# Kernel tuning notes

Measured on AMD Instinct MI355X. Metric: run time of the kernel, lower is better.

The kernel has to match this reference:

```python
import jax, jax.numpy as jnp
import numpy as np

NUM_NODES = 100000
NUM_RELATIONS = 16
HIDDEN = 64
NUM_LAYERS = 3
NUM_EDGES = 1600000


def setup_inputs() -> dict:
    key = jax.random.key(0)
    ks = jax.random.split(key, 6)
    edge_index = jax.random.randint(ks[0], (2, NUM_EDGES), 0, NUM_NODES, dtype=jnp.int64 if jax.config.jax_enable_x64 else jnp.int32)
    edge_type = jax.random.randint(ks[1], (NUM_EDGES,), 0, NUM_RELATIONS, dtype=edge_index.dtype)
    scale = 1.0 / np.sqrt(HIDDEN)
    node_emb = jax.random.normal(ks[2], (NUM_NODES, HIDDEN), dtype=jnp.float32) * scale
    # Per-layer relation weights [L, R, d, h], root weights [L, d, h], bias [L, h]
    W = jax.random.normal(ks[3], (NUM_LAYERS, NUM_RELATIONS, HIDDEN, HIDDEN), dtype=jnp.float32) * scale
    W_root = jax.random.normal(ks[4], (NUM_LAYERS, HIDDEN, HIDDEN), dtype=jnp.float32) * scale
    bias = jnp.zeros((NUM_LAYERS, HIDDEN), dtype=jnp.float32)
    return {"edge_index": edge_index, "edge_type": edge_type,
            "node_emb": node_emb, "W": W, "W_root": W_root, "bias": bias}


def _rgcn_layer(x, src, dst, et, Wr, Wroot, b):
    # PyG RGCNConv: out_i = W_root x_i + b + sum_r (1/|N_r(i)|) sum_{j in N_r(i)} W_r x_j
    N, d = x.shape
    R = Wr.shape[0]
    # Transform all nodes by every relation weight: [R, N, h] (dense grouped GEMM)
    xW = jnp.einsum('nd,rdh->rnh', x, Wr)
    m = xW[et, src]                      # [E, h] per-edge messages (gather)
    seg = dst * R + et                   # joint (dst, relation) segment id
    counts = jax.ops.segment_sum(jnp.ones((m.shape[0],), dtype=x.dtype), seg, num_segments=N * R)
    norm = 1.0 / jnp.maximum(counts, 1.0)
    m = m * norm[seg][:, None]           # per-relation mean normalization
    agg = jax.ops.segment_sum(m, dst, num_segments=N)  # scatter-add over dst
    return agg + x @ Wroot + b


def reference(edge_index, edge_type, node_emb, W, W_root, bias):
    src, dst = edge_index[0], edge_index[1]
    x = node_emb  # note: Embedding.max_norm only applies on index lookups; .weight used raw here
    n_layers = W.shape[0]
    for i in range(n_layers):
        x = _rgcn_layer(x, src, dst, edge_type, W[i], W_root[i], bias[i])
        if i < n_layers - 1:
            x = jax.nn.relu(x)
    return x
```

## Files before the change

kernel.cpp:

```cpp
#include <hip/hip_runtime.h>


#define HID   64
#define NREL  16
#define KD    1088
#define NPB   16
#define NPW   2
#define LSTR  1096

#define NBKT  1024
#define BSH   7
#define FB    2048
#define CAPB  4096
#define CHA   8192

typedef __attribute__((ext_vector_type(8))) short bf16x8;
typedef __attribute__((ext_vector_type(4))) float f32x4;
typedef unsigned short us16;
typedef unsigned int u32;

__device__ __forceinline__ float b2f(us16 u) {
    union { u32 i; float f; } c; c.i = ((u32)u) << 16; return c.f;
}
__device__ __forceinline__ us16 f2b(float f) {
    union { float f; u32 i; } c; c.f = f;
    u32 x = c.i;
    return (us16)((x + 0x7FFFu + ((x >> 16) & 1u)) >> 16);
}


__global__ __launch_bounds__(256) void bucket_count(const int* __restrict__ ei,
                                                    int* __restrict__ counts_b, int E) {
    __shared__ int h[NBKT];
    const int t = threadIdx.x;
    for (int i = t; i < NBKT; i += 256) h[i] = 0;
    __syncthreads();
    const int* dstp = ei + E;
    int start = blockIdx.x * CHA, end = min(start + CHA, E);
    for (int e4 = start + t * 4; e4 < end; e4 += 1024) {
        if (e4 + 3 < end) {
            int4 d = *(const int4*)(dstp + e4);
            atomicAdd(&h[d.x >> BSH], 1);
            atomicAdd(&h[d.y >> BSH], 1);
            atomicAdd(&h[d.z >> BSH], 1);
            atomicAdd(&h[d.w >> BSH], 1);
        } else {
            for (int e = e4; e < end; ++e) atomicAdd(&h[dstp[e] >> BSH], 1);
        }
    }
    __syncthreads();
    for (int i = t; i < NBKT; i += 256) {
        int v = h[i];
        if (v) atomicAdd(&counts_b[i], v);
    }
}

__global__ __launch_bounds__(NBKT) void scan_buckets(const int* __restrict__ counts_b,
                                                     int* __restrict__ bucket_base,
                                                     int* __restrict__ cursor_b,
                                                     int* __restrict__ row_ptr,
                                                     int N, int E) {
    __shared__ int s[NBKT];
    int t = threadIdx.x;
    int v = counts_b[t];
    s[t] = v; __syncthreads();
    for (int off = 1; off < NBKT; off <<= 1) {
        int tv = (t >= off) ? s[t - off] : 0;
        __syncthreads();
        s[t] += tv;
        __syncthreads();
    }
    int ex = s[t] - v;
    bucket_base[t] = ex;
    cursor_b[t] = ex;
    if (t == NBKT - 1) bucket_base[NBKT] = ex + v;
    if (t == 0) row_ptr[N] = E;
}

__global__ __launch_bounds__(256) void bucket_place(const int* __restrict__ ei,
                                                    const int* __restrict__ et,
                                                    int* __restrict__ cursor_b,
                                                    u32* __restrict__ packed, int E) {
    __shared__ int cnt[NBKT];
    __shared__ int bse[NBKT];
    const int t = threadIdx.x;
    for (int i = t; i < NBKT; i += 256) cnt[i] = 0;
    __syncthreads();
    const int* dstp = ei + E;
    int start = blockIdx.x * CHA, end = min(start + CHA, E);
    for (int e4 = start + t * 4; e4 < end; e4 += 1024) {
        if (e4 + 3 < end) {
            int4 d = *(const int4*)(dstp + e4);
            atomicAdd(&cnt[d.x >> BSH], 1);
            atomicAdd(&cnt[d.y >> BSH], 1);
            atomicAdd(&cnt[d.z >> BSH], 1);
            atomicAdd(&cnt[d.w >> BSH], 1);
        } else {
            for (int e = e4; e < end; ++e) atomicAdd(&cnt[dstp[e] >> BSH], 1);
        }
    }
    __syncthreads();
    for (int i = t; i < NBKT; i += 256) {
        int v = cnt[i];
        bse[i] = v ? atomicAdd(&cursor_b[i], v) : 0;
        cnt[i] = 0;
    }
    __syncthreads();
    #define PLACE1(sv, dv, tv)                                            \
        { int b_ = (dv) >> BSH;                                           \
          int r_ = atomicAdd(&cnt[b_], 1);                                \
          packed[bse[b_] + r_] = (u32)(sv) | ((u32)(tv) << 17)            \
                               | ((u32)((dv) & 127) << 21); }
    for (int e4 = start + t * 4; e4 < end; e4 += 1024) {
        if (e4 + 3 < end) {
            int4 sv = *(const int4*)(ei + e4);
            int4 dv = *(const int4*)(dstp + e4);
            int4 tv = *(const int4*)(et + e4);
            PLACE1(sv.x, dv.x, tv.x);
            PLACE1(sv.y, dv.y, tv.y);
            PLACE1(sv.z, dv.z, tv.z);
            PLACE1(sv.w, dv.w, tv.w);
        } else {
            for (int e = e4; e < end; ++e) PLACE1(ei[e], dstp[e], et[e]);
        }
    }
    #undef PLACE1
}

__global__ __launch_bounds__(256) void bucket_sort(const u32* __restrict__ packed,
                                                   const int* __restrict__ bucket_base,
                                                   u32* __restrict__ md,
                                                   int* __restrict__ row_ptr, int N) {
    __shared__ int hist[FB];
    __shared__ int ss[256];
    __shared__ u32 outb[CAPB];
    const int b = blockIdx.x, t = threadIdx.x;
    const int base = bucket_base[b];
    const int cnt = bucket_base[b + 1] - base;

    for (int i = t; i < FB; i += 256) hist[i] = 0;
    __syncthreads();
    for (int i = t; i < cnt; i += 256) {
        u32 p = packed[base + i];
        int f = (int)(((p >> 21) & 127u) * 16u + ((p >> 17) & 15u));
        atomicAdd(&hist[f], 1);
    }
    __syncthreads();
    int loc[8], s = 0;
    #pragma unroll
    for (int j = 0; j < 8; ++j) { loc[j] = hist[t * 8 + j]; s += loc[j]; }
    ss[t] = s; __syncthreads();
    for (int off = 1; off < 256; off <<= 1) {
        int tv = (t >= off) ? ss[t - off] : 0;
        __syncthreads();
        ss[t] += tv;
        __syncthreads();
    }
    int run = ss[t] - s;
    #pragma unroll
    for (int j = 0; j < 8; ++j) { hist[t * 8 + j] = run; run += loc[j]; }
    __syncthreads();
    if (t < 128) {
        int node = b * 128 + t;
        if (node < N) row_ptr[node] = base + hist[t * 16];
    }
    __syncthreads();
    for (int i = t; i < cnt; i += 256) {
        u32 p = packed[base + i];
        int f = (int)(((p >> 21) & 127u) * 16u + ((p >> 17) & 15u));
        int pos = atomicAdd(&hist[f], 1);
        u32 v = (p & 0x1FFFFu) | (((p >> 17) & 15u) << 20);
        if (pos < CAPB) outb[pos] = v;
        else            md[base + pos] = v;
    }
    __syncthreads();
    for (int i = t; i < cnt && i < CAPB; i += 256)
        md[base + i] = outb[i];
}

__global__ void convx_kernel(const float* __restrict__ x, us16* __restrict__ xb, int n4) {
    int i = blockIdx.x * 256 + threadIdx.x;
    if (i < n4) {
        float4 v = ((const float4*)x)[i];
        us16* o = xb + i * 4;
        o[0] = f2b(v.x); o[1] = f2b(v.y); o[2] = f2b(v.z); o[3] = f2b(v.w);
    }
}

__global__ void convw_kernel(const float* __restrict__ W, const float* __restrict__ Wroot,
                             us16* __restrict__ WcatT, int total, int L) {
    int i = blockIdx.x * 256 + threadIdx.x;
    if (i < total) {
        int l = i / (HID * KD);
        int rem = i % (HID * KD);
        int h = rem / KD, k = rem % KD;
        float v;
        if (k < NREL * HID) {
            int r = k >> 6, d = k & 63;
            v = W[(((size_t)l * NREL + r) * HID + d) * HID + h];
        } else {
            int d = k - NREL * HID;
            v = Wroot[((size_t)l * HID + d) * HID + h];
        }
        WcatT[i] = f2b(v);
    }
}


__device__ __forceinline__ void proc_window(
        u32 p_l, int c0, int wcnt, const us16* __restrict__ x_in, us16* Hrow, int lane,
        float& acc, int& runlen, int& prev, u32& mask)
{
    #pragma unroll 1
    for (int c = c0; c < wcnt; c += 16) {
        us16 hv[16]; int pe[16];
        #pragma unroll
        for (int j = 0; j < 16; ++j) {
            int idx = c + j; if (idx >= wcnt) idx = wcnt - 1;
            pe[j] = __builtin_amdgcn_readlane((int)p_l, idx);
            hv[j] = x_in[((u32)pe[j] & 0xFFFFFu) * HID + lane];
        }
        int m = wcnt - c; if (m > 16) m = 16;
        #pragma unroll
        for (int j = 0; j < 16; ++j) {
            if (j < m) {
                int r = (int)(((u32)pe[j]) >> 20);
                if (r != prev) {
                    if (prev >= 0) {
                        Hrow[(prev << 6) + lane] =
                            f2b(acc * __builtin_amdgcn_rcpf((float)runlen));
                        mask |= 1u << prev;
                    }
                    prev = r; acc = 0.f; runlen = 0;
                }
                acc += b2f(hv[j]); ++runlen;
            }
        }
    }
}

__global__ __launch_bounds__(512, 8) void layer_kernel(
        const us16* __restrict__ x_in,
        const int*  __restrict__ row_ptr,
        const u32*  __restrict__ md,
        const us16* __restrict__ WcatT,
        const float* __restrict__ bias,
        us16* __restrict__ x_out,
        float* __restrict__ out_f32,
        int flags, int N)
{
    __shared__ us16 H[NPB * LSTR];
    const int tid = threadIdx.x, wave = tid >> 6, lane = tid & 63;
    const int node0 = blockIdx.x * NPB;
    const int nodeq = node0 + wave * NPW;

    int rp[NPW + 1];
    #pragma unroll
    for (int i = 0; i <= NPW; ++i)
        rp[i] = __builtin_amdgcn_readfirstlane(row_ptr[min(nodeq + i, N)]);

    u32 pl[NPW]; us16 xr[NPW];
    #pragma unroll
    for (int q = 0; q < NPW; ++q) {
        int cnt = rp[q + 1] - rp[q];
        pl[q] = (lane < cnt) ? md[rp[q] + lane] : 0;
        xr[q] = (nodeq + q < N) ? x_in[(nodeq + q) * HID + lane] : (us16)0;
    }

    #pragma unroll
    for (int q = 0; q < NPW; ++q) {
        int node = nodeq + q;
        if (node >= N) break;
        int start = rp[q], cnt = rp[q + 1] - start;
        us16* Hrow = H + (wave * NPW + q) * LSTR;
        Hrow[NREL * HID + lane] = xr[q];

        float acc = 0.f;
        int runlen = 0, prev = -1;
        u32 mask = 0;

        proc_window(pl[q], 0, min(cnt, 64), x_in, Hrow, lane, acc, runlen, prev, mask);
        for (int w0 = 64; w0 < cnt; w0 += 64) {
            int wcnt = min(64, cnt - w0);
            u32 p2 = (lane < wcnt) ? md[start + w0 + lane] : 0;
            proc_window(p2, 0, wcnt, x_in, Hrow, lane, acc, runlen, prev, mask);
        }
        if (prev >= 0) {
            Hrow[(prev << 6) + lane] = f2b(acc * __builtin_amdgcn_rcpf((float)runlen));
            mask |= 1u << prev;
        }
        #pragma unroll
        for (int r = 0; r < NREL; ++r)
            if (!(mask & (1u << r))) Hrow[(r << 6) + lane] = 0;
    }
    __syncthreads();

    if (wave < 4) {
        const int n16 = lane & 15, quad = lane >> 4;
        f32x4 acc = {0.f, 0.f, 0.f, 0.f};
        const us16* Abase = H + n16 * LSTR + quad * 8;
        const us16* Bbase = WcatT + (size_t)(wave * 16 + n16) * KD + quad * 8;
        #pragma unroll 2
        for (int ks = 0; ks < KD / 32; ++ks) {
            bf16x8 af = *(const bf16x8*)(Abase + ks * 32);
            bf16x8 bf = *(const bf16x8*)(Bbase + ks * 32);
            acc = __builtin_amdgcn_mfma_f32_16x16x32_bf16(af, bf, acc, 0, 0, 0);
        }

        int col = wave * 16 + n16;
        float bv = bias[col];
        #pragma unroll
        for (int ri = 0; ri < 4; ++ri) {
            int nl = quad * 4 + ri, node = node0 + nl;
            if (node < N) {
                float v = acc[ri] + bv;
                if (flags & 1) v = fmaxf(v, 0.f);
                if (flags & 2) out_f32[node * HID + col] = v;
                else           x_out [node * HID + col] = f2b(v);
            }
        }
    }
}


extern "C" void kernel_launch(void* const* d_in, const int* in_sizes, int n_in,
                              void* d_out, int out_size, void* d_ws, size_t ws_size,
                              hipStream_t stream) {
    const int*   edge_index = (const int*)  d_in[0];
    const int*   edge_type  = (const int*)  d_in[1];
    const float* node_emb   = (const float*)d_in[2];
    const float* W          = (const float*)d_in[3];
    const float* Wroot      = (const float*)d_in[4];
    const float* bias       = (const float*)d_in[5];
    float* out = (float*)d_out;

    const int E = in_sizes[1];
    const int N = in_sizes[2] / HID;
    const int L = in_sizes[5] / HID;

    char* p = (char*)d_ws;
    size_t off = 0;
    auto carve = [&](size_t bytes) {
        void* q = p + off;
        off = (off + bytes + 255) & ~(size_t)255;
        return q;
    };
    int*   counts_b    = (int*)  carve((size_t)NBKT * 4);
    int*   bucket_base = (int*)  carve((size_t)(NBKT + 1) * 4);
    int*   cursor_b    = (int*)  carve((size_t)NBKT * 4);
    int*   row_ptr     = (int*)  carve((size_t)(N + 1) * 4);
    u32*   packed      = (u32*)  carve((size_t)E * 4);
    u32*   md          = (u32*)  carve((size_t)E * 4);
    us16*  xb0         = (us16*) carve((size_t)N * HID * 2);
    us16*  xb1         = (us16*) carve((size_t)N * HID * 2);
    us16*  WcatT       = (us16*) carve((size_t)L * HID * KD * 2);
    (void)ws_size; (void)n_in; (void)out_size;

    hipMemsetAsync(counts_b, 0, (size_t)NBKT * 4, stream);

    const int nblkA = (E + CHA - 1) / CHA;
    bucket_count<<<nblkA, 256, 0, stream>>>(edge_index, counts_b, E);
    scan_buckets<<<1, NBKT, 0, stream>>>(counts_b, bucket_base, cursor_b, row_ptr, N, E);
    bucket_place<<<nblkA, 256, 0, stream>>>(edge_index, edge_type, cursor_b, packed, E);
    bucket_sort<<<(N + 127) / 128, 256, 0, stream>>>(packed, bucket_base, md, row_ptr, N);

    convx_kernel<<<(N * HID / 4 + 255) / 256, 256, 0, stream>>>(node_emb, xb0, N * HID / 4);
    int wtot = L * HID * KD;
    convw_kernel<<<(wtot + 255) / 256, 256, 0, stream>>>(W, Wroot, WcatT, wtot, L);

    int gl = (N + NPB - 1) / NPB;
    us16* xin = xb0;
    us16* xother = xb1;
    for (int l = 0; l < L; ++l) {
        int last = (l == L - 1);
        int flags = (last ? 2 : 1);
        layer_kernel<<<gl, 512, 0, stream>>>(
            xin, row_ptr, md,
            WcatT + (size_t)l * HID * KD, bias + (size_t)l * HID,
            last ? nullptr : xother, last ? out : nullptr,
            flags, N);
        us16* t = xin; xin = xother; xother = t;
    }
}
```

Measured before the change: 535.0 us.

## Dynamically assign nodes to waves via shared-memory atomic work queue

Replaces the static two-nodes-per-wave assignment in the gather phase with a per-block LDS atomic counter. Each wave grabs the next node index and prefetches the following node's metadata and root row while it aggregates the current one. The goal is to balance uneven node degrees across the eight waves so the block waits less at the barrier before the MFMA stage. The cost is an extra barrier plus per-node LDS atomics and shuffles, and unrolled independent loads are traded for a software-pipelined loop.

```diff
diff --git a/kernel.cpp b/kernel.cpp
--- a/kernel.cpp
+++ b/kernel.cpp
@@ -5,7 +5,6 @@
 #define NREL  16
 #define KD    1088
 #define NPB   16
-#define NPW   2
 #define LSTR  1096
 
 #define NBKT  1024
@@ -250,48 +249,72 @@
         int flags, int N)
 {
     __shared__ us16 H[NPB * LSTR];
+    __shared__ int rp_s[NPB + 1];
+    __shared__ int qctr;
     const int tid = threadIdx.x, wave = tid >> 6, lane = tid & 63;
     const int node0 = blockIdx.x * NPB;
-    const int nodeq = node0 + wave * NPW;
-
-    int rp[NPW + 1];
-    #pragma unroll
-    for (int i = 0; i <= NPW; ++i)
-        rp[i] = __builtin_amdgcn_readfirstlane(row_ptr[min(nodeq + i, N)]);
-
-    u32 pl[NPW]; us16 xr[NPW];
-    #pragma unroll
-    for (int q = 0; q < NPW; ++q) {
-        int cnt = rp[q + 1] - rp[q];
-        pl[q] = (lane < cnt) ? md[rp[q] + lane] : 0;
-        xr[q] = (nodeq + q < N) ? x_in[(nodeq + q) * HID + lane] : (us16)0;
-    }
-
-    #pragma unroll
-    for (int q = 0; q < NPW; ++q) {
-        int node = nodeq + q;
-        if (node >= N) break;
-        int start = rp[q], cnt = rp[q + 1] - start;
-        us16* Hrow = H + (wave * NPW + q) * LSTR;
-        Hrow[NREL * HID + lane] = xr[q];
-
-        float acc = 0.f;
-        int runlen = 0, prev = -1;
-        u32 mask = 0;
-
-        proc_window(pl[q], 0, min(cnt, 64), x_in, Hrow, lane, acc, runlen, prev, mask);
-        for (int w0 = 64; w0 < cnt; w0 += 64) {
-            int wcnt = min(64, cnt - w0);
-            u32 p2 = (lane < wcnt) ? md[start + w0 + lane] : 0;
-            proc_window(p2, 0, wcnt, x_in, Hrow, lane, acc, runlen, prev, mask);
-        }
-        if (prev >= 0) {
-            Hrow[(prev << 6) + lane] = f2b(acc * __builtin_amdgcn_rcpf((float)runlen));
-            mask |= 1u << prev;
-        }
-        #pragma unroll
-        for (int r = 0; r < NREL; ++r)
-            if (!(mask & (1u << r))) Hrow[(r << 6) + lane] = 0;
+
+    if (tid <= NPB) rp_s[tid] = row_ptr[min(node0 + tid, N)];
+    if (tid == 0) qctr = 0;
+    __syncthreads();
+
+    {
+        int cA = 0;
+        if (lane == 0) cA = atomicAdd(&qctr, 1);
+        cA = __shfl(cA, 0);
+        int sA = 0, eA = 0; u32 plA = 0; us16 xrA = 0;
+        if (cA < NPB) {
+            sA = rp_s[cA]; eA = rp_s[cA + 1];
+            sA = __builtin_amdgcn_readfirstlane(sA);
+            eA = __builtin_amdgcn_readfirstlane(eA);
+            int cnt = eA - sA;
+            plA = (lane < cnt) ? md[sA + lane] : 0;
+            xrA = (node0 + cA < N) ? x_in[(size_t)(node0 + cA) * HID + lane] : (us16)0;
+        }
+
+        while (cA < NPB) {
+            int cB = 0;
+            if (lane == 0) cB = atomicAdd(&qctr, 1);
+            cB = __shfl(cB, 0);
+            int sB = 0, eB = 0; u32 plB = 0; us16 xrB = 0;
+            if (cB < NPB) {
+                sB = rp_s[cB]; eB = rp_s[cB + 1];
+                sB = __builtin_amdgcn_readfirstlane(sB);
+                eB = __builtin_amdgcn_readfirstlane(eB);
+                int cnt = eB - sB;
+                plB = (lane < cnt) ? md[sB + lane] : 0;
+                xrB = (node0 + cB < N) ? x_in[(size_t)(node0 + cB) * HID + lane] : (us16)0;
+            }
+
+            if (node0 + cA < N) {
+                int start = sA, cnt = eA - sA;
+                us16* Hrow = H + cA * LSTR;
+                Hrow[NREL * HID + lane] = xrA;
+
+                float acc = 0.f;
+                int runlen = 0, prev = -1;
+                u32 mask = 0;
+
+                proc_window(plA, 0, min(cnt, 64), x_in, Hrow, lane,
+                            acc, runlen, prev, mask);
+                for (int w0 = 64; w0 < cnt; w0 += 64) {
+                    int wcnt = min(64, cnt - w0);
+                    u32 p2 = (lane < wcnt) ? md[start + w0 + lane] : 0;
+                    proc_window(p2, 0, wcnt, x_in, Hrow, lane,
+                                acc, runlen, prev, mask);
+                }
+                if (prev >= 0) {
+                    Hrow[(prev << 6) + lane] =
+                        f2b(acc * __builtin_amdgcn_rcpf((float)runlen));
+                    mask |= 1u << prev;
+                }
+                #pragma unroll
+                for (int r = 0; r < NREL; ++r)
+                    if (!(mask & (1u << r))) Hrow[(r << 6) + lane] = 0;
+            }
+
+            cA = cB; sA = sB; eA = eB; plA = plB; xrA = xrB;
+        }
     }
     __syncthreads();
 
```

After: 569.3 us. 6.4% more time.

## Drop the bucket counting pass by placing edges into fixed-capacity buckets

Applied to the files above, without the earlier changes.

Removes the separate bucket_count kernel. Each of the 1024 buckets now gets a fixed 4096-slot region, so bucket_place can scatter packed edges directly, and the per-bucket cursors double as counts. The prefix scan runs after placement to produce compact bucket bases for bucket_sort. This saves one full read of the destination array and one launch, but uses a larger scratch buffer and silently overflows if any 128-node bucket receives more than 4096 edges, which only holds for fairly uniform graphs.

```diff
diff --git a/kernel.cpp b/kernel.cpp
--- a/kernel.cpp
+++ b/kernel.cpp
@@ -10,6 +10,7 @@
 
 #define NBKT  1024
 #define BSH   7
+#define BCAP  4096
 #define FB    2048
 #define CAPB  4096
 #define CHA   8192
@@ -28,54 +29,6 @@
     return (us16)((x + 0x7FFFu + ((x >> 16) & 1u)) >> 16);
 }
 
-
-__global__ __launch_bounds__(256) void bucket_count(const int* __restrict__ ei,
-                                                    int* __restrict__ counts_b, int E) {
-    __shared__ int h[NBKT];
-    const int t = threadIdx.x;
-    for (int i = t; i < NBKT; i += 256) h[i] = 0;
-    __syncthreads();
-    const int* dstp = ei + E;
-    int start = blockIdx.x * CHA, end = min(start + CHA, E);
-    for (int e4 = start + t * 4; e4 < end; e4 += 1024) {
-        if (e4 + 3 < end) {
-            int4 d = *(const int4*)(dstp + e4);
-            atomicAdd(&h[d.x >> BSH], 1);
-            atomicAdd(&h[d.y >> BSH], 1);
-            atomicAdd(&h[d.z >> BSH], 1);
-            atomicAdd(&h[d.w >> BSH], 1);
-        } else {
-            for (int e = e4; e < end; ++e) atomicAdd(&h[dstp[e] >> BSH], 1);
-        }
-    }
-    __syncthreads();
-    for (int i = t; i < NBKT; i += 256) {
-        int v = h[i];
-        if (v) atomicAdd(&counts_b[i], v);
-    }
-}
-
-__global__ __launch_bounds__(NBKT) void scan_buckets(const int* __restrict__ counts_b,
-                                                     int* __restrict__ bucket_base,
-                                                     int* __restrict__ cursor_b,
-                                                     int* __restrict__ row_ptr,
-                                                     int N, int E) {
-    __shared__ int s[NBKT];
-    int t = threadIdx.x;
-    int v = counts_b[t];
-    s[t] = v; __syncthreads();
-    for (int off = 1; off < NBKT; off <<= 1) {
-        int tv = (t >= off) ? s[t - off] : 0;
-        __syncthreads();
-        s[t] += tv;
-        __syncthreads();
-    }
-    int ex = s[t] - v;
-    bucket_base[t] = ex;
-    cursor_b[t] = ex;
-    if (t == NBKT - 1) bucket_base[NBKT] = ex + v;
-    if (t == 0) row_ptr[N] = E;
-}
 
 __global__ __launch_bounds__(256) void bucket_place(const int* __restrict__ ei,
                                                     const int* __restrict__ et,
@@ -102,7 +55,7 @@
     __syncthreads();
     for (int i = t; i < NBKT; i += 256) {
         int v = cnt[i];
-        bse[i] = v ? atomicAdd(&cursor_b[i], v) : 0;
+        bse[i] = v ? (i * BCAP + atomicAdd(&cursor_b[i], v)) : 0;
         cnt[i] = 0;
     }
     __syncthreads();
@@ -127,6 +80,26 @@
     #undef PLACE1
 }
 
+__global__ __launch_bounds__(NBKT) void scan_buckets(const int* __restrict__ cursor_b,
+                                                     int* __restrict__ bucket_base,
+                                                     int* __restrict__ row_ptr,
+                                                     int N, int E) {
+    __shared__ int s[NBKT];
+    int t = threadIdx.x;
+    int v = cursor_b[t];
+    s[t] = v; __syncthreads();
+    for (int off = 1; off < NBKT; off <<= 1) {
+        int tv = (t >= off) ? s[t - off] : 0;
+        __syncthreads();
+        s[t] += tv;
+        __syncthreads();
+    }
+    int ex = s[t] - v;
+    bucket_base[t] = ex;
+    if (t == NBKT - 1) bucket_base[NBKT] = ex + v;
+    if (t == 0) row_ptr[N] = E;
+}
+
 __global__ __launch_bounds__(256) void bucket_sort(const u32* __restrict__ packed,
                                                    const int* __restrict__ bucket_base,
                                                    u32* __restrict__ md,
@@ -137,11 +110,12 @@
     const int b = blockIdx.x, t = threadIdx.x;
     const int base = bucket_base[b];
     const int cnt = bucket_base[b + 1] - base;
+    const u32* pk = packed + (size_t)b * BCAP;
 
     for (int i = t; i < FB; i += 256) hist[i] = 0;
     __syncthreads();
     for (int i = t; i < cnt; i += 256) {
-        u32 p = packed[base + i];
+        u32 p = pk[i];
         int f = (int)(((p >> 21) & 127u) * 16u + ((p >> 17) & 15u));
         atomicAdd(&hist[f], 1);
     }
@@ -166,7 +140,7 @@
     }
     __syncthreads();
     for (int i = t; i < cnt; i += 256) {
-        u32 p = packed[base + i];
+        u32 p = pk[i];
         int f = (int)(((p >> 21) & 127u) * 16u + ((p >> 17) & 15u));
         int pos = atomicAdd(&hist[f], 1);
         u32 v = (p & 0x1FFFFu) | (((p >> 17) & 15u) << 20);
@@ -345,23 +319,21 @@
         off = (off + bytes + 255) & ~(size_t)255;
         return q;
     };
-    int*   counts_b    = (int*)  carve((size_t)NBKT * 4);
+    int*   cursor_b    = (int*)  carve((size_t)NBKT * 4);
     int*   bucket_base = (int*)  carve((size_t)(NBKT + 1) * 4);
-    int*   cursor_b    = (int*)  carve((size_t)NBKT * 4);
     int*   row_ptr     = (int*)  carve((size_t)(N + 1) * 4);
-    u32*   packed      = (u32*)  carve((size_t)E * 4);
+    u32*   packed      = (u32*)  carve((size_t)NBKT * BCAP * 4);
     u32*   md          = (u32*)  carve((size_t)E * 4);
     us16*  xb0         = (us16*) carve((size_t)N * HID * 2);
     us16*  xb1         = (us16*) carve((size_t)N * HID * 2);
     us16*  WcatT       = (us16*) carve((size_t)L * HID * KD * 2);
     (void)ws_size; (void)n_in; (void)out_size;
 
-    hipMemsetAsync(counts_b, 0, (size_t)NBKT * 4, stream);
+    hipMemsetAsync(cursor_b, 0, (size_t)NBKT * 4, stream);
 
     const int nblkA = (E + CHA - 1) / CHA;
-    bucket_count<<<nblkA, 256, 0, stream>>>(edge_index, counts_b, E);
-    scan_buckets<<<1, NBKT, 0, stream>>>(counts_b, bucket_base, cursor_b, row_ptr, N, E);
     bucket_place<<<nblkA, 256, 0, stream>>>(edge_index, edge_type, cursor_b, packed, E);
+    scan_buckets<<<1, NBKT, 0, stream>>>(cursor_b, bucket_base, row_ptr, N, E);
     bucket_sort<<<(N + 127) / 128, 256, 0, stream>>>(packed, bucket_base, md, row_ptr, N);
 
     convx_kernel<<<(N * HID / 4 + 255) / 256, 256, 0, stream>>>(node_emb, xb0, N * HID / 4);
```

Result: no change. 526.2 us, median of 2 (-1.6%).
